# Performance work log

Hardware: AMD Instinct MI355X
Metric: run time of the kernel (lower is better)

The kernel has to match this reference:

```python
import jax, jax.numpy as jnp
import numpy as np

B, N, D, HEADS, P, C = 64, 197, 768, 12, 12, 200
ARC_S, ARC_M = 30.0, 0.5


def layer_norm(x, g, b, eps=1e-5):
    m = jnp.mean(x, axis=-1, keepdims=True)
    v = jnp.var(x, axis=-1, keepdims=True)
    return (x - m) / jnp.sqrt(v + eps) * g + b


def setup_inputs() -> dict:
    key = jax.random.key(0)
    ks = jax.random.split(key, 16)
    sc = 0.02
    return {
        'hidden': jax.random.normal(ks[0], (B, N, D), jnp.float32),
        'attns': jax.random.uniform(ks[1], (4, B, HEADS, N, N), jnp.float32),
        'labels': jax.random.randint(ks[2], (B,), 0, C),
        'ln1_g': jnp.ones((D,), jnp.float32),
        'ln1_b': jnp.zeros((D,), jnp.float32),
        'w_in': jax.random.normal(ks[3], (3 * D, D), jnp.float32) * sc,
        'b_in': jnp.zeros((3 * D,), jnp.float32),
        'w_out': jax.random.normal(ks[4], (D, D), jnp.float32) * sc,
        'b_out': jnp.zeros((D,), jnp.float32),
        'ln2_g': jnp.ones((D,), jnp.float32),
        'ln2_b': jnp.zeros((D,), jnp.float32),
        'w_pool': jax.random.normal(ks[5], (1, D), jnp.float32) * sc,
        'b_pool': jnp.zeros((1,), jnp.float32),
        'pool_temp': jnp.float32(1.0),
        'w_mlp': jax.random.normal(ks[6], (D, D), jnp.float32) * sc,
        'b_mlp': jnp.zeros((D,), jnp.float32),
        'arc_w': jax.random.normal(ks[7], (C, 2 * D), jnp.float32) * sc,
    }


def reference(hidden, attns, labels, ln1_g, ln1_b, w_in, b_in, w_out, b_out,
              ln2_g, ln2_b, w_pool, b_pool, pool_temp, w_mlp, b_mlp, arc_w):
    cls_embed = hidden[:, 0]              # [B, D]
    patch_embeds = hidden[:, 1:]          # [B, N-1, D]

    # Multi-layer attention fusion: mean over heads, CLS row, drop CLS col.
    attn_scores = attns.mean(axis=2)[:, :, 0, 1:].mean(axis=0)  # [B, N-1]

    # Top-k part selection + gather.
    idx = jax.lax.top_k(attn_scores, P)[1]                       # [B, P]
    parts = jnp.take_along_axis(patch_embeds, idx[:, :, None], axis=1)  # [B,P,D]
    parts = layer_norm(parts, ln1_g, ln1_b)

    # Multi-head self-attention over parts (eval mode, no dropout).
    hd = D // HEADS
    qkv = parts @ w_in.T + b_in                                  # [B,P,3D]
    q, k, v = jnp.split(qkv, 3, axis=-1)
    def heads(t):
        return t.reshape(B, P, HEADS, hd).transpose(0, 2, 1, 3)  # [B,H,P,hd]
    q, k, v = heads(q), heads(k), heads(v)
    scores = jnp.einsum('bhqd,bhkd->bhqk', q, k) / jnp.sqrt(jnp.float32(hd))
    a = jax.nn.softmax(scores, axis=-1)
    o = jnp.einsum('bhqk,bhkd->bhqd', a, v)
    o = o.transpose(0, 2, 1, 3).reshape(B, P, D)
    attn_out = o @ w_out.T + b_out
    attn_out = layer_norm(attn_out, ln2_g, ln2_b)

    # Temperature-softmax weighted pooling.
    raw_w = (attn_out @ w_pool.T + b_pool)[..., 0]               # [B,P]
    weights = jax.nn.softmax(raw_w / jnp.maximum(pool_temp, 0.3), axis=1)
    part_feat = jnp.sum(attn_out * weights[..., None], axis=1)   # [B,D]
    part_feat = jax.nn.relu(part_feat @ w_mlp.T + b_mlp)

    fusion = jnp.concatenate([cls_embed, part_feat], axis=1)     # [B,2D]

    # ArcFace margin (train logits with labels).
    fn = fusion / jnp.linalg.norm(fusion, axis=-1, keepdims=True)
    wn = arc_w / jnp.linalg.norm(arc_w, axis=-1, keepdims=True)
    cosine = fn @ wn.T                                           # [B,C]
    sine = jnp.sqrt(jnp.clip(1.0 - cosine ** 2, 0.0, 1.0))
    cos_m, sin_m = np.cos(ARC_M), np.sin(ARC_M)
    th = np.cos(np.pi - ARC_M)
    mm = np.sin(np.pi - ARC_M) * ARC_M
    phi = cosine * cos_m - sine * sin_m
    phi = jnp.where(cosine > th, phi, cosine - mm)
    one_hot = jax.nn.one_hot(labels, C, dtype=cosine.dtype)
    logits = (one_hot * phi + (1.0 - one_hot) * cosine) * ARC_S
    return logits
```

## Files before the change

kernel.cpp:

```cpp
#include <hip/hip_runtime.h>
#include <hip/hip_bf16.h>
#include <float.h>
#include <math.h>

#define BB 64
#define NNtok 197
#define DD 768
#define HH 12
#define PP 12
#define CC 200
#define NPATCH 196

typedef short bf16x8 __attribute__((ext_vector_type(8)));
typedef float f32x4 __attribute__((ext_vector_type(4)));

__device__ __forceinline__ unsigned short bf16_bits(float x) {
  __hip_bfloat16 h = __float2bfloat16(x);
  return *reinterpret_cast<unsigned short*>(&h);
}
__device__ __forceinline__ float bf16u_val(unsigned short us) {
  union { unsigned int u; float f; } cv;
  cv.u = ((unsigned int)us) << 16;
  return cv.f;
}
__device__ __forceinline__ float bf16_val(const __hip_bfloat16* p) {
  return __bfloat162float(*p);
}

__global__ __launch_bounds__(256) void k_front(
    const float* __restrict__ hidden, const float* __restrict__ attns,
    const float* __restrict__ g, const float* __restrict__ be,
    const float* __restrict__ w1, const float* __restrict__ w2,
    const float* __restrict__ w3, __hip_bfloat16* __restrict__ o1,
    __hip_bfloat16* __restrict__ o2, __hip_bfloat16* __restrict__ o3,
    __hip_bfloat16* __restrict__ parts) {
  int t = threadIdx.x;
  int bi = blockIdx.x;
  if (bi >= 64) {
    int i = (bi - 64) * 256 + t;
    const float* src; __hip_bfloat16* dst; int off;
    if (i < 442368) { src = w1; dst = o1; off = i; }
    else if (i < 589824) { src = w2; dst = o2; off = i - 442368; }
    else { src = w3; dst = o3; off = i - 589824; }
    float4 v = ((const float4*)src)[off];
    union { unsigned short u[4]; ushort4 v4; } p;
    p.u[0] = bf16_bits(v.x); p.u[1] = bf16_bits(v.y);
    p.u[2] = bf16_bits(v.z); p.u[3] = bf16_bits(v.w);
    ((ushort4*)dst)[off] = p.v4;
    return;
  }
  int b = bi;
  __shared__ float sc[256];
  __shared__ int sel_s[PP];
  float acc = -FLT_MAX;
  if (t < NPATCH) {
    acc = 0.f;
#pragma unroll
    for (int l = 0; l < 4; l++) {
      float part = 0.f;
#pragma unroll
      for (int h = 0; h < HH; h++) {
        size_t base = (size_t)((l * BB + b) * HH + h) * ((size_t)NNtok * NNtok);
        part += attns[base + 1 + t];
      }
      acc += part * (1.f / 12.f);
    }
    acc *= 0.25f;
  }
  sc[t] = acc;
  __syncthreads();
  if (t < 64) {
    float v[4]; int idx[4];
#pragma unroll
    for (int j = 0; j < 4; j++) { idx[j] = t + j * 64; v[j] = sc[idx[j]]; }
    for (int it = 0; it < PP; ++it) {
      float bv = v[0]; int bidx = idx[0];
#pragma unroll
      for (int j = 1; j < 4; j++)
        if (v[j] > bv || (v[j] == bv && idx[j] < bidx)) { bv = v[j]; bidx = idx[j]; }
      float cv = bv; int ci = bidx;
#pragma unroll
      for (int off = 32; off > 0; off >>= 1) {
        float ov = __shfl_xor(cv, off); int oi = __shfl_xor(ci, off);
        if (ov > cv || (ov == cv && oi < ci)) { cv = ov; ci = oi; }
      }
      if (t == 0) sel_s[it] = ci;
#pragma unroll
      for (int j = 0; j < 4; j++)
        if (idx[j] == ci) v[j] = -FLT_MAX;
    }
  }
  __syncthreads();
  int wv = t >> 6, ln = t & 63;
#pragma unroll
  for (int q = 0; q < 3; q++) {
    int i = wv * 3 + q;
    const float* row = hidden + ((size_t)b * NNtok + 1 + sel_s[i]) * DD;
    float x[12], s1 = 0.f, s2 = 0.f;
#pragma unroll
    for (int k = 0; k < 12; k++) {
      x[k] = row[ln + 64 * k];
      s1 += x[k]; s2 += x[k] * x[k];
    }
#pragma unroll
    for (int off = 32; off > 0; off >>= 1) {
      s1 += __shfl_xor(s1, off); s2 += __shfl_xor(s2, off);
    }
    float m = s1 * (1.f / DD);
    float rstd = rsqrtf(s2 * (1.f / DD) - m * m + 1e-5f);
    __hip_bfloat16* out = parts + ((size_t)b * PP + i) * DD;
#pragma unroll
    for (int k = 0; k < 12; k++) {
      int d = ln + 64 * k;
      out[d] = __float2bfloat16((x[k] - m) * rstd * g[d] + be[d]);
    }
  }
}

template <int MI, int NJ, int WM, int WN, int RELU, int OUTBF>
__global__ __launch_bounds__(WM * WN * 64) void k_gemm_bf(
    const __hip_bfloat16* __restrict__ A, const __hip_bfloat16* __restrict__ W,
    const float* __restrict__ bias, void* __restrict__ Cd, int Nn, int Kk) {
  int t = threadIdx.x;
  int wave = t >> 6, lane = t & 63;
  int wm = wave / WN, wn = wave % WN;
  int row0 = blockIdx.y * (WM * MI * 16) + wm * MI * 16;
  int col0 = blockIdx.x * (WN * NJ * 16) + wn * NJ * 16;
  int lr = lane & 15;
  int kg = lane >> 4;
  f32x4 acc[MI][NJ];
#pragma unroll
  for (int i = 0; i < MI; i++)
#pragma unroll
    for (int j = 0; j < NJ; j++) {
      acc[i][j][0] = 0.f; acc[i][j][1] = 0.f;
      acc[i][j][2] = 0.f; acc[i][j][3] = 0.f;
    }
  const __hip_bfloat16* Ab = A + (size_t)(row0 + lr) * Kk + kg * 8;
  const __hip_bfloat16* Wb = W + (size_t)(col0 + lr) * Kk + kg * 8;
  for (int k0 = 0; k0 < Kk; k0 += 32) {
    bf16x8 af[MI], wf[NJ];
#pragma unroll
    for (int i = 0; i < MI; i++)
      af[i] = *(const bf16x8*)(Ab + (size_t)i * 16 * Kk + k0);
#pragma unroll
    for (int j = 0; j < NJ; j++)
      wf[j] = *(const bf16x8*)(Wb + (size_t)j * 16 * Kk + k0);
#pragma unroll
    for (int i = 0; i < MI; i++)
#pragma unroll
      for (int j = 0; j < NJ; j++)
        acc[i][j] = __builtin_amdgcn_mfma_f32_16x16x32_bf16(af[i], wf[j],
                                                            acc[i][j], 0, 0, 0);
  }
#pragma unroll
  for (int i = 0; i < MI; i++) {
#pragma unroll
    for (int j = 0; j < NJ; j++) {
      int r0 = row0 + i * 16 + kg * 4;
      int c = col0 + j * 16 + lr;
      float bv = bias[c];
#pragma unroll
      for (int r = 0; r < 4; r++) {
        float v = acc[i][j][r] + bv;
        if (RELU) v = fmaxf(v, 0.f);
        if (OUTBF)
          ((__hip_bfloat16*)Cd)[(size_t)(r0 + r) * Nn + c] = __float2bfloat16(v);
        else
          ((float*)Cd)[(size_t)(r0 + r) * Nn + c] = v;
      }
    }
  }
}

__global__ __launch_bounds__(256) void k_attn(
    const __hip_bfloat16* __restrict__ qkv, __hip_bfloat16* __restrict__ o) {
  int bh = blockIdx.x;
  int b = bh / HH, h = bh % HH;
  __shared__ float qs[12][64], ks[12][64], vs[12][64], sm[12][12];
  int t = threadIdx.x;
  for (int u = t; u < 768; u += 256) {
    int p = u >> 6, d = u & 63;
    size_t base = ((size_t)(b * PP + p)) * 2304 + h * 64 + d;
    qs[p][d] = bf16_val(qkv + base);
    ks[p][d] = bf16_val(qkv + base + 768);
    vs[p][d] = bf16_val(qkv + base + 1536);
  }
  __syncthreads();
  if (t < 144) {
    int i = t / 12, j = t % 12;
    float s = 0.f;
#pragma unroll
    for (int d = 0; d < 64; d++) s += qs[i][d] * ks[j][d];
    sm[i][j] = s * 0.125f;
  }
  __syncthreads();
  if (t < 12) {
    float m = -FLT_MAX;
    for (int j = 0; j < 12; j++) m = fmaxf(m, sm[t][j]);
    float e[12], sum = 0.f;
    for (int j = 0; j < 12; j++) { e[j] = expf(sm[t][j] - m); sum += e[j]; }
    float inv = 1.f / sum;
    for (int j = 0; j < 12; j++) sm[t][j] = e[j] * inv;
  }
  __syncthreads();
  for (int u = t; u < 768; u += 256) {
    int i = u >> 6, d = u & 63;
    float s = 0.f;
#pragma unroll
    for (int j = 0; j < 12; j++) s += sm[i][j] * vs[j][d];
    o[((size_t)(b * PP + i)) * DD + h * 64 + d] = __float2bfloat16(s);
  }
}

__global__ __launch_bounds__(256) void k_head(
    const float* __restrict__ aout, const float* __restrict__ g,
    const float* __restrict__ be, const float* __restrict__ wp,
    const float* __restrict__ bp, const float* __restrict__ ptemp,
    const __hip_bfloat16* __restrict__ wmlp, const float* __restrict__ bmlp,
    float* __restrict__ pmlp) {
  int b = blockIdx.x, t = threadIdx.x, wv = t >> 6, ln = t & 63;
  __shared__ float ybuf[12][768];
  __shared__ float raww_s[12];
  __shared__ float pfeat_s[768];
#pragma unroll
  for (int q = 0; q < 3; q++) {
    int r = wv * 3 + q;
    const float* row = aout + ((size_t)(b * PP + r)) * DD;
    float x[12], s1 = 0.f, s2 = 0.f;
#pragma unroll
    for (int k = 0; k < 12; k++) {
      x[k] = row[ln + 64 * k];
      s1 += x[k]; s2 += x[k] * x[k];
    }
#pragma unroll
    for (int off = 32; off > 0; off >>= 1) {
      s1 += __shfl_xor(s1, off); s2 += __shfl_xor(s2, off);
    }
    float m = s1 * (1.f / DD);
    float rstd = rsqrtf(s2 * (1.f / DD) - m * m + 1e-5f);
    float pl = 0.f;
#pragma unroll
    for (int k = 0; k < 12; k++) {
      int d = ln + 64 * k;
      float y = (x[k] - m) * rstd * g[d] + be[d];
      ybuf[r][d] = y;
      pl += y * wp[d];
    }
#pragma unroll
    for (int off = 32; off > 0; off >>= 1) pl += __shfl_xor(pl, off);
    if (ln == 0) raww_s[r] = pl + bp[0];
  }
  __syncthreads();
  float wts[12];
  {
    float inv = 1.f / fmaxf(ptemp[0], 0.3f);
    float z[12], mx = -FLT_MAX;
#pragma unroll
    for (int p = 0; p < 12; p++) { z[p] = raww_s[p] * inv; mx = fmaxf(mx, z[p]); }
    float s = 0.f;
#pragma unroll
    for (int p = 0; p < 12; p++) { z[p] = expf(z[p] - mx); s += z[p]; }
    float is = 1.f / s;
#pragma unroll
    for (int p = 0; p < 12; p++) wts[p] = z[p] * is;
  }
  for (int d = t; d < DD; d += 256) {
    float s = 0.f;
#pragma unroll
    for (int p = 0; p < 12; p++) s += ybuf[p][d] * wts[p];
    pfeat_s[d] = s;
  }
  __syncthreads();
  for (int j = t; j < DD; j += 256) {
    const bf16x8* wr = (const bf16x8*)(wmlp + (size_t)j * DD);
    float acc2 = bmlp[j];
    for (int k = 0; k < 96; k++) {
      bf16x8 w8 = wr[k];
      const float* pf = &pfeat_s[k * 8];
#pragma unroll
      for (int e = 0; e < 8; e++)
        acc2 += pf[e] * bf16u_val((unsigned short)w8[e]);
    }
    pmlp[(size_t)b * DD + j] = fmaxf(acc2, 0.f);
  }
}

__global__ __launch_bounds__(256) void k_arc3(
    const float* __restrict__ hidden, const float* __restrict__ pmlp,
    const float* __restrict__ aw, const int* __restrict__ labels,
    float* __restrict__ out) {
  int b = blockIdx.y, t = threadIdx.x;
  __shared__ float4 fs[384];
  __shared__ float a4[4];
  const float4* cls4 = (const float4*)(hidden + (size_t)b * NNtok * DD);
  const float4* pm4 = (const float4*)(pmlp + (size_t)b * DD);
  for (int u = t; u < 384; u += 256) fs[u] = (u < 192) ? cls4[u] : pm4[u - 192];
  __syncthreads();
  float s = 0.f;
  for (int u = t; u < 384; u += 256) {
    float4 v = fs[u];
    s += v.x * v.x + v.y * v.y + v.z * v.z + v.w * v.w;
  }
#pragma unroll
  for (int off = 32; off > 0; off >>= 1) s += __shfl_xor(s, off);
  if ((t & 63) == 0) a4[t >> 6] = s;
  __syncthreads();
  float rnf = rsqrtf(a4[0] + a4[1] + a4[2] + a4[3]);
  int wv = t >> 6, ln = t & 63;
  int lab = labels[b];
  const float cos_m = 0.8775825618903728f, sin_m = 0.479425538604203f;
  const float th = -0.8775825618903728f, mm = 0.2397127693021015f;
#pragma unroll
  for (int ci = 0; ci < 2; ci++) {
    int c = blockIdx.x * 8 + wv + ci * 4;
    const float4* wr = (const float4*)(aw + (size_t)c * 1536);
    float acc = 0.f, nw = 0.f;
#pragma unroll
    for (int k = 0; k < 6; k++) {
      float4 a = fs[ln + 64 * k];
      float4 w = wr[ln + 64 * k];
      acc += a.x * w.x + a.y * w.y + a.z * w.z + a.w * w.w;
      nw += w.x * w.x + w.y * w.y + w.z * w.z + w.w * w.w;
    }
#pragma unroll
    for (int off = 32; off > 0; off >>= 1) {
      acc += __shfl_xor(acc, off); nw += __shfl_xor(nw, off);
    }
    if (ln == 0) {
      float cosv = acc * rsqrtf(nw) * rnf;
      float s2 = 1.f - cosv * cosv;
      s2 = fminf(fmaxf(s2, 0.f), 1.f);
      float sinv = sqrtf(s2);
      float phi = cosv * cos_m - sinv * sin_m;
      phi = (cosv > th) ? phi : (cosv - mm);
      out[(size_t)b * CC + c] = ((c == lab) ? phi : cosv) * 30.f;
    }
  }
}

extern "C" void kernel_launch(void* const* d_in, const int* in_sizes, int n_in,
                              void* d_out, int out_size, void* d_ws, size_t ws_size,
                              hipStream_t stream) {
  const float* hidden = (const float*)d_in[0];
  const float* attns  = (const float*)d_in[1];
  const int*   labels = (const int*)d_in[2];
  const float* ln1_g  = (const float*)d_in[3];
  const float* ln1_b  = (const float*)d_in[4];
  const float* w_in   = (const float*)d_in[5];
  const float* b_in   = (const float*)d_in[6];
  const float* w_out  = (const float*)d_in[7];
  const float* b_out  = (const float*)d_in[8];
  const float* ln2_g  = (const float*)d_in[9];
  const float* ln2_b  = (const float*)d_in[10];
  const float* w_pool = (const float*)d_in[11];
  const float* b_pool = (const float*)d_in[12];
  const float* ptemp  = (const float*)d_in[13];
  const float* w_mlp  = (const float*)d_in[14];
  const float* b_mlp  = (const float*)d_in[15];
  const float* arc_w  = (const float*)d_in[16];
  float* outp = (float*)d_out;

  float* F = (float*)d_ws;
  float* reg1 = F;
  float* pmlp = F + 884736;
  __hip_bfloat16* parts_bf = (__hip_bfloat16*)(F + 933888);
  __hip_bfloat16* w_in_bf  = (__hip_bfloat16*)(F + 1228800);
  __hip_bfloat16* w_out_bf = (__hip_bfloat16*)(F + 2113536);
  __hip_bfloat16* w_mlp_bf = (__hip_bfloat16*)(F + 2408448);
  __hip_bfloat16* qkv_bf = (__hip_bfloat16*)reg1;
  float* aout = reg1;
  __hip_bfloat16* obuf_bf = parts_bf;

  k_front<<<2944, 256, 0, stream>>>(hidden, attns, ln1_g, ln1_b,
                                    w_in, w_out, w_mlp,
                                    w_in_bf, w_out_bf, w_mlp_bf, parts_bf);
  k_gemm_bf<2, 4, 4, 1, 0, 1><<<dim3(36, 6), 256, 0, stream>>>(
      parts_bf, w_in_bf, b_in, (void*)qkv_bf, 2304, 768);
  k_attn<<<BB * HH, 256, 0, stream>>>(qkv_bf, obuf_bf);
  k_gemm_bf<2, 2, 2, 2, 0, 0><<<dim3(12, 12), 256, 0, stream>>>(
      obuf_bf, w_out_bf, b_out, (void*)aout, 768, 768);
  k_head<<<BB, 256, 0, stream>>>(aout, ln2_g, ln2_b, w_pool, b_pool, ptemp,
                                 w_mlp_bf, b_mlp, pmlp);
  k_arc3<<<dim3(25, BB), 256, 0, stream>>>(hidden, pmlp, arc_w, labels, outp);
}
```

Baseline: 105.4 us.

## Fuse pipeline into one cooperative persistent kernel with grid syncs

Result: slower. 395.3 us (+275.1%).

```diff
diff --git a/kernel.cpp b/kernel.cpp
--- a/kernel.cpp
+++ b/kernel.cpp
@@ -1,7 +1,10 @@
 #include <hip/hip_runtime.h>
+#include <hip/hip_cooperative_groups.h>
 #include <hip/hip_bf16.h>
 #include <float.h>
 #include <math.h>
+
+namespace cg = cooperative_groups;
 
 #define BB 64
 #define NNtok 197
@@ -10,6 +13,7 @@
 #define PP 12
 #define CC 200
 #define NPATCH 196
+#define SMB 21632
 
 typedef short bf16x8 __attribute__((ext_vector_type(8)));
 typedef float f32x4 __attribute__((ext_vector_type(4)));
@@ -18,24 +22,383 @@
   __hip_bfloat16 h = __float2bfloat16(x);
   return *reinterpret_cast<unsigned short*>(&h);
 }
-__device__ __forceinline__ float bf16u_val(unsigned short us) {
-  union { unsigned int u; float f; } cv;
-  cv.u = ((unsigned int)us) << 16;
-  return cv.f;
+__device__ __forceinline__ float u2f(unsigned int u) {
+  union { unsigned int u; float f; } cv; cv.u = u; return cv.f;
 }
 __device__ __forceinline__ float bf16_val(const __hip_bfloat16* p) {
   return __bfloat162float(*p);
 }
 
-__global__ __launch_bounds__(256) void k_front(
+template <int RELU, int OUTBF>
+__device__ __forceinline__ void gemm_tile64(
+    const __hip_bfloat16* __restrict__ A, const __hip_bfloat16* __restrict__ W,
+    const float* __restrict__ bias, void* __restrict__ Cd, int Nn, int Kk,
+    int mt, int nt, int t) {
+  int wave = t >> 6, lane = t & 63;
+  int wm = wave >> 1, wn = wave & 1;
+  int row0 = mt * 64 + wm * 32;
+  int col0 = nt * 64 + wn * 32;
+  int lr = lane & 15;
+  int kg = lane >> 4;
+  f32x4 acc[2][2];
+#pragma unroll
+  for (int i = 0; i < 2; i++)
+#pragma unroll
+    for (int j = 0; j < 2; j++) {
+      acc[i][j][0] = 0.f; acc[i][j][1] = 0.f;
+      acc[i][j][2] = 0.f; acc[i][j][3] = 0.f;
+    }
+  const __hip_bfloat16* Ab = A + (size_t)(row0 + lr) * Kk + kg * 8;
+  const __hip_bfloat16* Wb = W + (size_t)(col0 + lr) * Kk + kg * 8;
+  for (int k0 = 0; k0 < Kk; k0 += 32) {
+    bf16x8 af[2], wf[2];
+#pragma unroll
+    for (int i = 0; i < 2; i++)
+      af[i] = *(const bf16x8*)(Ab + (size_t)i * 16 * Kk + k0);
+#pragma unroll
+    for (int j = 0; j < 2; j++)
+      wf[j] = *(const bf16x8*)(Wb + (size_t)j * 16 * Kk + k0);
+#pragma unroll
+    for (int i = 0; i < 2; i++)
+#pragma unroll
+      for (int j = 0; j < 2; j++)
+        acc[i][j] = __builtin_amdgcn_mfma_f32_16x16x32_bf16(af[i], wf[j],
+                                                            acc[i][j], 0, 0, 0);
+  }
+#pragma unroll
+  for (int i = 0; i < 2; i++) {
+#pragma unroll
+    for (int j = 0; j < 2; j++) {
+      int r0 = row0 + i * 16 + kg * 4;
+      int c = col0 + j * 16 + lr;
+      float bv = bias[c];
+#pragma unroll
+      for (int r = 0; r < 4; r++) {
+        float v = acc[i][j][r] + bv;
+        if (RELU) v = fmaxf(v, 0.f);
+        if (OUTBF)
+          ((__hip_bfloat16*)Cd)[(size_t)(r0 + r) * Nn + c] = __float2bfloat16(v);
+        else
+          ((float*)Cd)[(size_t)(r0 + r) * Nn + c] = v;
+      }
+    }
+  }
+}
+
+__device__ __forceinline__ void dev_select_ln1(
+    int b, int t, const float* __restrict__ hidden,
+    const float* __restrict__ attns, const float* __restrict__ g,
+    const float* __restrict__ be, __hip_bfloat16* __restrict__ parts,
+    char* smraw) {
+  float* sc = (float*)smraw;
+  int* sel_s = (int*)(smraw + 1024);
+  int wv = t >> 6, ln = t & 63;
+  float acc = -FLT_MAX;
+  if (t < NPATCH) {
+    acc = 0.f;
+#pragma unroll
+    for (int l = 0; l < 4; l++) {
+      float part = 0.f;
+#pragma unroll
+      for (int h = 0; h < HH; h++) {
+        size_t base = (size_t)((l * BB + b) * HH + h) * ((size_t)NNtok * NNtok);
+        part += attns[base + 1 + t];
+      }
+      acc += part * (1.f / 12.f);
+    }
+    acc *= 0.25f;
+  }
+  sc[t] = acc;
+  __syncthreads();
+  if (t < 64) {
+    float v[4]; int idx[4];
+#pragma unroll
+    for (int j = 0; j < 4; j++) { idx[j] = t + j * 64; v[j] = sc[idx[j]]; }
+    for (int it = 0; it < PP; ++it) {
+      float bv = v[0]; int bidx = idx[0];
+#pragma unroll
+      for (int j = 1; j < 4; j++)
+        if (v[j] > bv || (v[j] == bv && idx[j] < bidx)) { bv = v[j]; bidx = idx[j]; }
+      float cv = bv; int ci = bidx;
+#pragma unroll
+      for (int off = 32; off > 0; off >>= 1) {
+        float ov = __shfl_xor(cv, off); int oi = __shfl_xor(ci, off);
+        if (ov > cv || (ov == cv && oi < ci)) { cv = ov; ci = oi; }
+      }
+      if (t == 0) sel_s[it] = ci;
+#pragma unroll
+      for (int j = 0; j < 4; j++)
+        if (idx[j] == ci) v[j] = -FLT_MAX;
+    }
+  }
+  __syncthreads();
+#pragma unroll
+  for (int q = 0; q < 3; q++) {
+    int i = wv * 3 + q;
+    const float* row = hidden + ((size_t)b * NNtok + 1 + sel_s[i]) * DD;
+    float x[12], s1 = 0.f, s2 = 0.f;
+#pragma unroll
+    for (int k = 0; k < 12; k++) {
+      x[k] = row[ln + 64 * k];
+      s1 += x[k]; s2 += x[k] * x[k];
+    }
+#pragma unroll
+    for (int off = 32; off > 0; off >>= 1) {
+      s1 += __shfl_xor(s1, off); s2 += __shfl_xor(s2, off);
+    }
+    float m = s1 * (1.f / DD);
+    float rstd = rsqrtf(s2 * (1.f / DD) - m * m + 1e-5f);
+    __hip_bfloat16* outp_ = parts + ((size_t)b * PP + i) * DD;
+#pragma unroll
+    for (int k = 0; k < 12; k++) {
+      int d = ln + 64 * k;
+      outp_[d] = __float2bfloat16((x[k] - m) * rstd * g[d] + be[d]);
+    }
+  }
+}
+
+__device__ __forceinline__ void dev_attn(
+    int task, int t, const __hip_bfloat16* __restrict__ qkv,
+    __hip_bfloat16* __restrict__ o, char* smraw) {
+  float* qs = (float*)smraw;
+  float* ks = qs + 768;
+  float* vs = ks + 768;
+  float* smx = vs + 768;
+  int b = task / HH, h = task % HH;
+  for (int u = t; u < 768; u += 256) {
+    int p = u >> 6, d = u & 63;
+    size_t base = ((size_t)(b * PP + p)) * 2304 + h * 64 + d;
+    qs[u] = bf16_val(qkv + base);
+    ks[u] = bf16_val(qkv + base + 768);
+    vs[u] = bf16_val(qkv + base + 1536);
+  }
+  __syncthreads();
+  if (t < 144) {
+    int i = t / 12, j = t % 12;
+    float s = 0.f;
+#pragma unroll
+    for (int d = 0; d < 64; d++) s += qs[i * 64 + d] * ks[j * 64 + d];
+    smx[i * 12 + j] = s * 0.125f;
+  }
+  __syncthreads();
+  if (t < 12) {
+    float m = -FLT_MAX;
+    for (int j = 0; j < 12; j++) m = fmaxf(m, smx[t * 12 + j]);
+    float e[12], sum = 0.f;
+    for (int j = 0; j < 12; j++) { e[j] = expf(smx[t * 12 + j] - m); sum += e[j]; }
+    float inv = 1.f / sum;
+    for (int j = 0; j < 12; j++) smx[t * 12 + j] = e[j] * inv;
+  }
+  __syncthreads();
+  for (int u = t; u < 768; u += 256) {
+    int i = u >> 6, d = u & 63;
+    float s = 0.f;
+#pragma unroll
+    for (int j = 0; j < 12; j++) s += smx[i * 12 + j] * vs[j * 64 + d];
+    o[((size_t)(b * PP + i)) * DD + h * 64 + d] = __float2bfloat16(s);
+  }
+  __syncthreads();
+}
+
+__device__ __forceinline__ void dev_head(
+    int b, int t, const float* __restrict__ aout, const float* __restrict__ g,
+    const float* __restrict__ be, const float* __restrict__ wp,
+    const float* __restrict__ bp, const float* __restrict__ ptemp,
+    const __hip_bfloat16* __restrict__ wmlp, const float* __restrict__ bmlp,
+    float* __restrict__ pmlp, char* smraw) {
+  int wv = t >> 6, ln = t & 63;
+  __hip_bfloat16* ybuf = (__hip_bfloat16*)smraw;
+  float* raww_s = (float*)(smraw + 18432);
+  float* pfeat = (float*)(smraw + 18496);
+#pragma unroll
+  for (int q = 0; q < 3; q++) {
+    int r = wv * 3 + q;
+    const float* row = aout + ((size_t)(b * PP + r)) * DD;
+    float x[12], s1 = 0.f, s2 = 0.f;
+#pragma unroll
+    for (int k = 0; k < 12; k++) {
+      x[k] = row[ln + 64 * k];
+      s1 += x[k]; s2 += x[k] * x[k];
+    }
+#pragma unroll
+    for (int off = 32; off > 0; off >>= 1) {
+      s1 += __shfl_xor(s1, off); s2 += __shfl_xor(s2, off);
+    }
+    float m = s1 * (1.f / DD);
+    float rstd = rsqrtf(s2 * (1.f / DD) - m * m + 1e-5f);
+    float pl = 0.f;
+#pragma unroll
+    for (int k = 0; k < 12; k++) {
+      int d = ln + 64 * k;
+      float y = (x[k] - m) * rstd * g[d] + be[d];
+      ybuf[r * 768 + d] = __float2bfloat16(y);
+      pl += y * wp[d];
+    }
+#pragma unroll
+    for (int off = 32; off > 0; off >>= 1) pl += __shfl_xor(pl, off);
+    if (ln == 0) raww_s[r] = pl + bp[0];
+  }
+  __syncthreads();
+  float wts[12];
+  {
+    float inv = 1.f / fmaxf(ptemp[0], 0.3f);
+    float z[12], mx = -FLT_MAX;
+#pragma unroll
+    for (int p = 0; p < 12; p++) { z[p] = raww_s[p] * inv; mx = fmaxf(mx, z[p]); }
+    float s = 0.f;
+#pragma unroll
+    for (int p = 0; p < 12; p++) { z[p] = expf(z[p] - mx); s += z[p]; }
+    float is = 1.f / s;
+#pragma unroll
+    for (int p = 0; p < 12; p++) wts[p] = z[p] * is;
+  }
+  for (int d = t; d < DD; d += 256) {
+    float s = 0.f;
+#pragma unroll
+    for (int p = 0; p < 12; p++) s += __bfloat162float(ybuf[p * 768 + d]) * wts[p];
+    pfeat[d] = s;
+  }
+  __syncthreads();
+  for (int j = t; j < DD; j += 256) {
+    const uint4* wr = (const uint4*)(wmlp + (size_t)j * DD);
+    float acc2 = bmlp[j];
+    for (int k = 0; k < 96; k++) {
+      uint4 w4 = wr[k];
+      const float* pf = &pfeat[k * 8];
+      acc2 += pf[0] * u2f(w4.x << 16) + pf[1] * u2f(w4.x & 0xFFFF0000u)
+            + pf[2] * u2f(w4.y << 16) + pf[3] * u2f(w4.y & 0xFFFF0000u)
+            + pf[4] * u2f(w4.z << 16) + pf[5] * u2f(w4.z & 0xFFFF0000u)
+            + pf[6] * u2f(w4.w << 16) + pf[7] * u2f(w4.w & 0xFFFF0000u);
+    }
+    pmlp[(size_t)b * DD + j] = fmaxf(acc2, 0.f);
+  }
+  __syncthreads();
+}
+
+__device__ __forceinline__ float dev_arc_load(
+    int b, int t, const float* __restrict__ hidden,
+    const float* __restrict__ pmlp, char* smraw) {
+  float4* fs4 = (float4*)smraw;
+  float* a4 = (float*)(smraw + 6144);
+  int wv = t >> 6, ln = t & 63;
+  const float4* cls4 = (const float4*)(hidden + (size_t)b * NNtok * DD);
+  const float4* pm4 = (const float4*)(pmlp + (size_t)b * DD);
+  for (int u = t; u < 384; u += 256) fs4[u] = (u < 192) ? cls4[u] : pm4[u - 192];
+  __syncthreads();
+  float s = 0.f;
+  for (int u = t; u < 384; u += 256) {
+    float4 v = fs4[u];
+    s += v.x * v.x + v.y * v.y + v.z * v.z + v.w * v.w;
+  }
+#pragma unroll
+  for (int off = 32; off > 0; off >>= 1) s += __shfl_xor(s, off);
+  if (ln == 0) a4[wv] = s;
+  __syncthreads();
+  return rsqrtf(a4[0] + a4[1] + a4[2] + a4[3]);
+}
+
+__device__ __forceinline__ void dev_arc_cblk(
+    int cblk, int b, float rnf, int t, const float* __restrict__ aw,
+    const int* __restrict__ labels, float* __restrict__ out, char* smraw) {
+  float4* fs4 = (float4*)smraw;
+  int wv = t >> 6, ln = t & 63;
+  int lab = labels[b];
+  const float cos_m = 0.8775825618903728f, sin_m = 0.479425538604203f;
+  const float th = -0.8775825618903728f, mm = 0.2397127693021015f;
+#pragma unroll
+  for (int ci = 0; ci < 2; ci++) {
+    int c = cblk * 8 + wv + ci * 4;
+    const float4* wr = (const float4*)(aw + (size_t)c * 1536);
+    float acc = 0.f, nw = 0.f;
+#pragma unroll
+    for (int k = 0; k < 6; k++) {
+      float4 a = fs4[ln + 64 * k];
+      float4 w = wr[ln + 64 * k];
+      acc += a.x * w.x + a.y * w.y + a.z * w.z + a.w * w.w;
+      nw += w.x * w.x + w.y * w.y + w.z * w.z + w.w * w.w;
+    }
+#pragma unroll
+    for (int off = 32; off > 0; off >>= 1) {
+      acc += __shfl_xor(acc, off); nw += __shfl_xor(nw, off);
+    }
+    if (ln == 0) {
+      float cosv = acc * rsqrtf(nw) * rnf;
+      float s2 = 1.f - cosv * cosv;
+      s2 = fminf(fmaxf(s2, 0.f), 1.f);
+      float sinv = sqrtf(s2);
+      float phi = cosv * cos_m - sinv * sin_m;
+      phi = (cosv > th) ? phi : (cosv - mm);
+      out[(size_t)b * CC + c] = ((c == lab) ? phi : cosv) * 30.f;
+    }
+  }
+}
+
+__global__ __launch_bounds__(256) void k_mega(
+    const float* __restrict__ hidden, const float* __restrict__ attns,
+    const int* __restrict__ labels, const float* __restrict__ ln1_g,
+    const float* __restrict__ ln1_b, const float* __restrict__ w_in,
+    const float* __restrict__ b_in, const float* __restrict__ w_out,
+    const float* __restrict__ b_out, const float* __restrict__ ln2_g,
+    const float* __restrict__ ln2_b, const float* __restrict__ w_pool,
+    const float* __restrict__ b_pool, const float* __restrict__ ptemp,
+    const float* __restrict__ w_mlp, const float* __restrict__ b_mlp,
+    const float* __restrict__ arc_w, float* __restrict__ out,
+    __hip_bfloat16* __restrict__ w_in_bf, __hip_bfloat16* __restrict__ w_out_bf,
+    __hip_bfloat16* __restrict__ w_mlp_bf, __hip_bfloat16* __restrict__ parts_bf,
+    __hip_bfloat16* __restrict__ qkv_bf, __hip_bfloat16* __restrict__ obuf_bf,
+    float* __restrict__ aout, float* __restrict__ pmlp) {
+  cg::grid_group gg = cg::this_grid();
+  __shared__ __align__(16) char smraw[SMB];
+  int t = threadIdx.x, blk = blockIdx.x, nb = gridDim.x;
+
+  if (blk < 64) {
+    dev_select_ln1(blk, t, hidden, attns, ln1_g, ln1_b, parts_bf, smraw);
+  } else {
+    for (int i = (blk - 64) * 256 + t; i < 737280; i += (nb - 64) * 256) {
+      const float* src; __hip_bfloat16* dst; int off;
+      if (i < 442368) { src = w_in; dst = w_in_bf; off = i; }
+      else if (i < 589824) { src = w_out; dst = w_out_bf; off = i - 442368; }
+      else { src = w_mlp; dst = w_mlp_bf; off = i - 589824; }
+      float4 v = ((const float4*)src)[off];
+      union { unsigned short u[4]; ushort4 v4; } p;
+      p.u[0] = bf16_bits(v.x); p.u[1] = bf16_bits(v.y);
+      p.u[2] = bf16_bits(v.z); p.u[3] = bf16_bits(v.w);
+      ((ushort4*)dst)[off] = p.v4;
+    }
+  }
+  gg.sync();
+  for (int tile = blk; tile < 432; tile += nb)
+    gemm_tile64<0, 1>(parts_bf, w_in_bf, b_in, (void*)qkv_bf, 2304, 768,
+                      tile % 12, tile / 12, t);
+  gg.sync();
+  for (int task = blk; task < 768; task += nb)
+    dev_attn(task, t, qkv_bf, obuf_bf, smraw);
+  gg.sync();
+  for (int tile = blk; tile < 144; tile += nb)
+    gemm_tile64<0, 0>(obuf_bf, w_out_bf, b_out, (void*)aout, 768, 768,
+                      tile % 12, tile / 12, t);
+  gg.sync();
+  for (int b = blk; b < 64; b += nb)
+    dev_head(b, t, aout, ln2_g, ln2_b, w_pool, b_pool, ptemp, w_mlp_bf, b_mlp,
+             pmlp, smraw);
+  gg.sync();
+  {
+    int b = blk & 63;
+    float rnf = dev_arc_load(b, t, hidden, pmlp, smraw);
+    for (int cblk = blk >> 6; cblk < 25; cblk += (nb >> 6))
+      dev_arc_cblk(cblk, b, rnf, t, arc_w, labels, out, smraw);
+  }
+}
+
+__global__ __launch_bounds__(256) void kf_front(
     const float* __restrict__ hidden, const float* __restrict__ attns,
     const float* __restrict__ g, const float* __restrict__ be,
     const float* __restrict__ w1, const float* __restrict__ w2,
     const float* __restrict__ w3, __hip_bfloat16* __restrict__ o1,
     __hip_bfloat16* __restrict__ o2, __hip_bfloat16* __restrict__ o3,
     __hip_bfloat16* __restrict__ parts) {
-  int t = threadIdx.x;
-  int bi = blockIdx.x;
+  __shared__ __align__(16) char smraw[2048];
+  int t = threadIdx.x, bi = blockIdx.x;
   if (bi >= 64) {
     int i = (bi - 64) * 256 + t;
     const float* src; __hip_bfloat16* dst; int off;
@@ -49,294 +412,42 @@
     ((ushort4*)dst)[off] = p.v4;
     return;
   }
-  int b = bi;
-  __shared__ float sc[256];
-  __shared__ int sel_s[PP];
-  float acc = -FLT_MAX;
-  if (t < NPATCH) {
-    acc = 0.f;
-#pragma unroll
-    for (int l = 0; l < 4; l++) {
-      float part = 0.f;
-#pragma unroll
-      for (int h = 0; h < HH; h++) {
-        size_t base = (size_t)((l * BB + b) * HH + h) * ((size_t)NNtok * NNtok);
-        part += attns[base + 1 + t];
-      }
-      acc += part * (1.f / 12.f);
-    }
-    acc *= 0.25f;
-  }
-  sc[t] = acc;
-  __syncthreads();
-  if (t < 64) {
-    float v[4]; int idx[4];
-#pragma unroll
-    for (int j = 0; j < 4; j++) { idx[j] = t + j * 64; v[j] = sc[idx[j]]; }
-    for (int it = 0; it < PP; ++it) {
-      float bv = v[0]; int bidx = idx[0];
-#pragma unroll
-      for (int j = 1; j < 4; j++)
-        if (v[j] > bv || (v[j] == bv && idx[j] < bidx)) { bv = v[j]; bidx = idx[j]; }
-      float cv = bv; int ci = bidx;
-#pragma unroll
-      for (int off = 32; off > 0; off >>= 1) {
-        float ov = __shfl_xor(cv, off); int oi = __shfl_xor(ci, off);
-        if (ov > cv || (ov == cv && oi < ci)) { cv = ov; ci = oi; }
-      }
-      if (t == 0) sel_s[it] = ci;
-#pragma unroll
-      for (int j = 0; j < 4; j++)
-        if (idx[j] == ci) v[j] = -FLT_MAX;
-    }
-  }
-  __syncthreads();
-  int wv = t >> 6, ln = t & 63;
-#pragma unroll
-  for (int q = 0; q < 3; q++) {
-    int i = wv * 3 + q;
-    const float* row = hidden + ((size_t)b * NNtok + 1 + sel_s[i]) * DD;
-    float x[12], s1 = 0.f, s2 = 0.f;
-#pragma unroll
-    for (int k = 0; k < 12; k++) {
-      x[k] = row[ln + 64 * k];
-      s1 += x[k]; s2 += x[k] * x[k];
-    }
-#pragma unroll
-    for (int off = 32; off > 0; off >>= 1) {
-      s1 += __shfl_xor(s1, off); s2 += __shfl_xor(s2, off);
-    }
-    float m = s1 * (1.f / DD);
-    float rstd = rsqrtf(s2 * (1.f / DD) - m * m + 1e-5f);
-    __hip_bfloat16* out = parts + ((size_t)b * PP + i) * DD;
-#pragma unroll
-    for (int k = 0; k < 12; k++) {
-      int d = ln + 64 * k;
-      out[d] = __float2bfloat16((x[k] - m) * rstd * g[d] + be[d]);
-    }
-  }
-}
-
-template <int MI, int NJ, int WM, int WN, int RELU, int OUTBF>
-__global__ __launch_bounds__(WM * WN * 64) void k_gemm_bf(
+  dev_select_ln1(bi, t, hidden, attns, g, be, parts, smraw);
+}
+
+template <int RELU, int OUTBF>
+__global__ __launch_bounds__(256) void kf_gemm(
     const __hip_bfloat16* __restrict__ A, const __hip_bfloat16* __restrict__ W,
     const float* __restrict__ bias, void* __restrict__ Cd, int Nn, int Kk) {
-  int t = threadIdx.x;
-  int wave = t >> 6, lane = t & 63;
-  int wm = wave / WN, wn = wave % WN;
-  int row0 = blockIdx.y * (WM * MI * 16) + wm * MI * 16;
-  int col0 = blockIdx.x * (WN * NJ * 16) + wn * NJ * 16;
-  int lr = lane & 15;
-  int kg = lane >> 4;
-  f32x4 acc[MI][NJ];
-#pragma unroll
-  for (int i = 0; i < MI; i++)
-#pragma unroll
-    for (int j = 0; j < NJ; j++) {
-      acc[i][j][0] = 0.f; acc[i][j][1] = 0.f;
-      acc[i][j][2] = 0.f; acc[i][j][3] = 0.f;
-    }
-  const __hip_bfloat16* Ab = A + (size_t)(row0 + lr) * Kk + kg * 8;
-  const __hip_bfloat16* Wb = W + (size_t)(col0 + lr) * Kk + kg * 8;
-  for (int k0 = 0; k0 < Kk; k0 += 32) {
-    bf16x8 af[MI], wf[NJ];
-#pragma unroll
-    for (int i = 0; i < MI; i++)
-      af[i] = *(const bf16x8*)(Ab + (size_t)i * 16 * Kk + k0);
-#pragma unroll
-    for (int j = 0; j < NJ; j++)
-      wf[j] = *(const bf16x8*)(Wb + (size_t)j * 16 * Kk + k0);
-#pragma unroll
-    for (int i = 0; i < MI; i++)
-#pragma unroll
-      for (int j = 0; j < NJ; j++)
-        acc[i][j] = __builtin_amdgcn_mfma_f32_16x16x32_bf16(af[i], wf[j],
-                                                            acc[i][j], 0, 0, 0);
-  }
-#pragma unroll
-  for (int i = 0; i < MI; i++) {
-#pragma unroll
-    for (int j = 0; j < NJ; j++) {
-      int r0 = row0 + i * 16 + kg * 4;
-      int c = col0 + j * 16 + lr;
-      float bv = bias[c];
-#pragma unroll
-      for (int r = 0; r < 4; r++) {
-        float v = acc[i][j][r] + bv;
-        if (RELU) v = fmaxf(v, 0.f);
-        if (OUTBF)
-          ((__hip_bfloat16*)Cd)[(size_t)(r0 + r) * Nn + c] = __float2bfloat16(v);
-        else
-          ((float*)Cd)[(size_t)(r0 + r) * Nn + c] = v;
-      }
-    }
-  }
-}
-
-__global__ __launch_bounds__(256) void k_attn(
+  gemm_tile64<RELU, OUTBF>(A, W, bias, Cd, Nn, Kk, blockIdx.y, blockIdx.x,
+                           threadIdx.x);
+}
+
+__global__ __launch_bounds__(256) void kf_attn(
     const __hip_bfloat16* __restrict__ qkv, __hip_bfloat16* __restrict__ o) {
-  int bh = blockIdx.x;
-  int b = bh / HH, h = bh % HH;
-  __shared__ float qs[12][64], ks[12][64], vs[12][64], sm[12][12];
-  int t = threadIdx.x;
-  for (int u = t; u < 768; u += 256) {
-    int p = u >> 6, d = u & 63;
-    size_t base = ((size_t)(b * PP + p)) * 2304 + h * 64 + d;
-    qs[p][d] = bf16_val(qkv + base);
-    ks[p][d] = bf16_val(qkv + base + 768);
-    vs[p][d] = bf16_val(qkv + base + 1536);
-  }
-  __syncthreads();
-  if (t < 144) {
-    int i = t / 12, j = t % 12;
-    float s = 0.f;
-#pragma unroll
-    for (int d = 0; d < 64; d++) s += qs[i][d] * ks[j][d];
-    sm[i][j] = s * 0.125f;
-  }
-  __syncthreads();
-  if (t < 12) {
-    float m = -FLT_MAX;
-    for (int j = 0; j < 12; j++) m = fmaxf(m, sm[t][j]);
-    float e[12], sum = 0.f;
-    for (int j = 0; j < 12; j++) { e[j] = expf(sm[t][j] - m); sum += e[j]; }
-    float inv = 1.f / sum;
-    for (int j = 0; j < 12; j++) sm[t][j] = e[j] * inv;
-  }
-  __syncthreads();
-  for (int u = t; u < 768; u += 256) {
-    int i = u >> 6, d = u & 63;
-    float s = 0.f;
-#pragma unroll
-    for (int j = 0; j < 12; j++) s += sm[i][j] * vs[j][d];
-    o[((size_t)(b * PP + i)) * DD + h * 64 + d] = __float2bfloat16(s);
-  }
-}
-
-__global__ __launch_bounds__(256) void k_head(
+  __shared__ __align__(16) char smraw[9792];
+  dev_attn(blockIdx.x, threadIdx.x, qkv, o, smraw);
+}
+
+__global__ __launch_bounds__(256) void kf_head(
     const float* __restrict__ aout, const float* __restrict__ g,
     const float* __restrict__ be, const float* __restrict__ wp,
     const float* __restrict__ bp, const float* __restrict__ ptemp,
     const __hip_bfloat16* __restrict__ wmlp, const float* __restrict__ bmlp,
     float* __restrict__ pmlp) {
-  int b = blockIdx.x, t = threadIdx.x, wv = t >> 6, ln = t & 63;
-  __shared__ float ybuf[12][768];
-  __shared__ float raww_s[12];
-  __shared__ float pfeat_s[768];
-#pragma unroll
-  for (int q = 0; q < 3; q++) {
-    int r = wv * 3 + q;
-    const float* row = aout + ((size_t)(b * PP + r)) * DD;
-    float x[12], s1 = 0.f, s2 = 0.f;
-#pragma unroll
-    for (int k = 0; k < 12; k++) {
-      x[k] = row[ln + 64 * k];
-      s1 += x[k]; s2 += x[k] * x[k];
-    }
-#pragma unroll
-    for (int off = 32; off > 0; off >>= 1) {
-      s1 += __shfl_xor(s1, off); s2 += __shfl_xor(s2, off);
-    }
-    float m = s1 * (1.f / DD);
-    float rstd = rsqrtf(s2 * (1.f / DD) - m * m + 1e-5f);
-    float pl = 0.f;
-#pragma unroll
-    for (int k = 0; k < 12; k++) {
-      int d = ln + 64 * k;
-      float y = (x[k] - m) * rstd * g[d] + be[d];
-      ybuf[r][d] = y;
-      pl += y * wp[d];
-    }
-#pragma unroll
-    for (int off = 32; off > 0; off >>= 1) pl += __shfl_xor(pl, off);
-    if (ln == 0) raww_s[r] = pl + bp[0];
-  }
-  __syncthreads();
-  float wts[12];
-  {
-    float inv = 1.f / fmaxf(ptemp[0], 0.3f);
-    float z[12], mx = -FLT_MAX;
-#pragma unroll
-    for (int p = 0; p < 12; p++) { z[p] = raww_s[p] * inv; mx = fmaxf(mx, z[p]); }
-    float s = 0.f;
-#pragma unroll
-    for (int p = 0; p < 12; p++) { z[p] = expf(z[p] - mx); s += z[p]; }
-    float is = 1.f / s;
-#pragma unroll
-    for (int p = 0; p < 12; p++) wts[p] = z[p] * is;
-  }
-  for (int d = t; d < DD; d += 256) {
-    float s = 0.f;
-#pragma unroll
-    for (int p = 0; p < 12; p++) s += ybuf[p][d] * wts[p];
-    pfeat_s[d] = s;
-  }
-  __syncthreads();
-  for (int j = t; j < DD; j += 256) {
-    const bf16x8* wr = (const bf16x8*)(wmlp + (size_t)j * DD);
-    float acc2 = bmlp[j];
-    for (int k = 0; k < 96; k++) {
-      bf16x8 w8 = wr[k];
-      const float* pf = &pfeat_s[k * 8];
-#pragma unroll
-      for (int e = 0; e < 8; e++)
-        acc2 += pf[e] * bf16u_val((unsigned short)w8[e]);
-    }
-    pmlp[(size_t)b * DD + j] = fmaxf(acc2, 0.f);
-  }
-}
-
-__global__ __launch_bounds__(256) void k_arc3(
+  __shared__ __align__(16) char smraw[SMB];
+  dev_head(blockIdx.x, threadIdx.x, aout, g, be, wp, bp, ptemp, wmlp, bmlp,
+           pmlp, smraw);
+}
+
+__global__ __launch_bounds__(256) void kf_arc(
     const float* __restrict__ hidden, const float* __restrict__ pmlp,
     const float* __restrict__ aw, const int* __restrict__ labels,
     float* __restrict__ out) {
+  __shared__ __align__(16) char smraw[6208];
   int b = blockIdx.y, t = threadIdx.x;
-  __shared__ float4 fs[384];
-  __shared__ float a4[4];
-  const float4* cls4 = (const float4*)(hidden + (size_t)b * NNtok * DD);
-  const float4* pm4 = (const float4*)(pmlp + (size_t)b * DD);
-  for (int u = t; u < 384; u += 256) fs[u] = (u < 192) ? cls4[u] : pm4[u - 192];
-  __syncthreads();
-  float s = 0.f;
-  for (int u = t; u < 384; u += 256) {
-    float4 v = fs[u];
-    s += v.x * v.x + v.y * v.y + v.z * v.z + v.w * v.w;
-  }
-#pragma unroll
-  for (int off = 32; off > 0; off >>= 1) s += __shfl_xor(s, off);
-  if ((t & 63) == 0) a4[t >> 6] = s;
-  __syncthreads();
-  float rnf = rsqrtf(a4[0] + a4[1] + a4[2] + a4[3]);
-  int wv = t >> 6, ln = t & 63;
-  int lab = labels[b];
-  const float cos_m = 0.8775825618903728f, sin_m = 0.479425538604203f;
-  const float th = -0.8775825618903728f, mm = 0.2397127693021015f;
-#pragma unroll
-  for (int ci = 0; ci < 2; ci++) {
-    int c = blockIdx.x * 8 + wv + ci * 4;
-    const float4* wr = (const float4*)(aw + (size_t)c * 1536);
-    float acc = 0.f, nw = 0.f;
-#pragma unroll
-    for (int k = 0; k < 6; k++) {
-      float4 a = fs[ln + 64 * k];
-      float4 w = wr[ln + 64 * k];
-      acc += a.x * w.x + a.y * w.y + a.z * w.z + a.w * w.w;
-      nw += w.x * w.x + w.y * w.y + w.z * w.z + w.w * w.w;
-    }
-#pragma unroll
-    for (int off = 32; off > 0; off >>= 1) {
-      acc += __shfl_xor(acc, off); nw += __shfl_xor(nw, off);
-    }
-    if (ln == 0) {
-      float cosv = acc * rsqrtf(nw) * rnf;
-      float s2 = 1.f - cosv * cosv;
-      s2 = fminf(fmaxf(s2, 0.f), 1.f);
-      float sinv = sqrtf(s2);
-      float phi = cosv * cos_m - sinv * sin_m;
-      phi = (cosv > th) ? phi : (cosv - mm);
-      out[(size_t)b * CC + c] = ((c == lab) ? phi : cosv) * 30.f;
-    }
-  }
+  float rnf = dev_arc_load(b, t, hidden, pmlp, smraw);
+  dev_arc_cblk(blockIdx.x, b, rnf, t, aw, labels, out, smraw);
 }
 
 extern "C" void kernel_launch(void* const* d_in, const int* in_sizes, int n_in,
@@ -372,15 +483,40 @@
   float* aout = reg1;
   __hip_bfloat16* obuf_bf = parts_bf;
 
-  k_front<<<2944, 256, 0, stream>>>(hidden, attns, ln1_g, ln1_b,
-                                    w_in, w_out, w_mlp,
-                                    w_in_bf, w_out_bf, w_mlp_bf, parts_bf);
-  k_gemm_bf<2, 4, 4, 1, 0, 1><<<dim3(36, 6), 256, 0, stream>>>(
-      parts_bf, w_in_bf, b_in, (void*)qkv_bf, 2304, 768);
-  k_attn<<<BB * HH, 256, 0, stream>>>(qkv_bf, obuf_bf);
-  k_gemm_bf<2, 2, 2, 2, 0, 0><<<dim3(12, 12), 256, 0, stream>>>(
-      obuf_bf, w_out_bf, b_out, (void*)aout, 768, 768);
-  k_head<<<BB, 256, 0, stream>>>(aout, ln2_g, ln2_b, w_pool, b_pool, ptemp,
-                                 w_mlp_bf, b_mlp, pmlp);
-  k_arc3<<<dim3(25, BB), 256, 0, stream>>>(hidden, pmlp, arc_w, labels, outp);
-}
+  int dev = 0;
+  hipGetDevice(&dev);
+  int nCU = 256;
+  hipDeviceGetAttribute(&nCU, hipDeviceAttributeMultiprocessorCount, dev);
+  int occ = 0;
+  hipOccupancyMaxActiveBlocksPerMultiprocessor(&occ, (const void*)k_mega, 256, 0);
+  long cap = (long)occ * (long)nCU;
+  int grid = (int)(cap > 512 ? 512 : cap);
+  grid = (grid / 64) * 64;
+
+  hipError_t rc = hipErrorUnknown;
+  if (grid >= 128) {
+    void* args[] = {
+        (void*)&hidden, (void*)&attns, (void*)&labels, (void*)&ln1_g,
+        (void*)&ln1_b, (void*)&w_in, (void*)&b_in, (void*)&w_out,
+        (void*)&b_out, (void*)&ln2_g, (void*)&ln2_b, (void*)&w_pool,
+        (void*)&b_pool, (void*)&ptemp, (void*)&w_mlp, (void*)&b_mlp,
+        (void*)&arc_w, (void*)&outp, (void*)&w_in_bf, (void*)&w_out_bf,
+        (void*)&w_mlp_bf, (void*)&parts_bf, (void*)&qkv_bf, (void*)&obuf_bf,
+        (void*)&aout, (void*)&pmlp};
+    rc = hipLaunchCooperativeKernel((void*)k_mega, dim3(grid), dim3(256), args,
+                                    0, stream);
+  }
+  if (rc != hipSuccess) {
+    kf_front<<<2944, 256, 0, stream>>>(hidden, attns, ln1_g, ln1_b, w_in, w_out,
+                                       w_mlp, w_in_bf, w_out_bf, w_mlp_bf,
+                                       parts_bf);
+    kf_gemm<0, 1><<<dim3(36, 12), 256, 0, stream>>>(parts_bf, w_in_bf, b_in,
+                                                    (void*)qkv_bf, 2304, 768);
+    kf_attn<<<768, 256, 0, stream>>>(qkv_bf, obuf_bf);
+    kf_gemm<0, 0><<<dim3(12, 12), 256, 0, stream>>>(obuf_bf, w_out_bf, b_out,
+                                                    (void*)aout, 768, 768);
+    kf_head<<<64, 256, 0, stream>>>(aout, ln2_g, ln2_b, w_pool, b_pool, ptemp,
+                                    w_mlp_bf, b_mlp, pmlp);
+    kf_arc<<<dim3(25, 64), 256, 0, stream>>>(hidden, pmlp, arc_w, labels, outp);
+  }
+}
```
